# Performance work log

Measured on AMD Instinct MI355X. Metric: run time of the kernel, lower is better.

## Reference

```python
import jax, jax.numpy as jnp
import numpy as np

NEG = -1e9  # stand-in for -inf in masked_fill; avoids NaN rows for never-gathered states


def _residual(x, w1, b1, w2, b2):
    # ResidualLayerOld: two relu linears with a residual connection (eval mode, no dropout)
    h = jax.nn.relu(x @ w1.T + b1)
    return x + jax.nn.relu(h @ w2.T + b2)


def setup_inputs() -> dict:
    key = jax.random.key(0)
    B, T, V, C, H, SPW = 16, 256, 32000, 1024, 512, 8
    ks = jax.random.split(key, 32)
    s = 0.05  # keep logits in a sane range
    inp = {
        'start_emb': jax.random.normal(ks[0], (C, H), jnp.float32) * s,
        'start_l1w': jax.random.normal(ks[1], (H, H), jnp.float32) * s,
        'start_l1b': jnp.zeros((H,), jnp.float32),
        'start_l2w': jax.random.normal(ks[2], (H, H), jnp.float32) * s,
        'start_l2b': jnp.zeros((H,), jnp.float32),
        'start_ow': jax.random.normal(ks[3], (1, H), jnp.float32) * s,
        'start_ob': jnp.zeros((1,), jnp.float32),
        'state_emb': jax.random.normal(ks[4], (C, H), jnp.float32) * s,
        'trans_l1w': jax.random.normal(ks[5], (H, H), jnp.float32) * s,
        'trans_l1b': jnp.zeros((H,), jnp.float32),
        'trans_l2w': jax.random.normal(ks[6], (H, H), jnp.float32) * s,
        'trans_l2b': jnp.zeros((H,), jnp.float32),
        'proj_w': jax.random.normal(ks[7], (C, H), jnp.float32) * s,
        'pret_emb': jax.random.normal(ks[8], (C, H), jnp.float32) * s,
        'term_l1w': jax.random.normal(ks[9], (H, H), jnp.float32) * s,
        'term_l1b': jnp.zeros((H,), jnp.float32),
        'term_l2w': jax.random.normal(ks[10], (H, H), jnp.float32) * s,
        'term_l2b': jnp.zeros((H,), jnp.float32),
        'term_ow': jax.random.normal(ks[11], (V, H), jnp.float32) * s,
        'term_ob': jnp.zeros((V,), jnp.float32),
        'text': jax.random.randint(ks[12], (B, T), 0, V, jnp.int32),
        'word2state': jax.random.randint(ks[13], (V, SPW), 0, C, jnp.int32),
    }
    return inp


def reference(start_emb, start_l1w, start_l1b, start_l2w, start_l2b, start_ow, start_ob,
              state_emb, trans_l1w, trans_l1b, trans_l2w, trans_l2b, proj_w,
              pret_emb, term_l1w, term_l1b, term_l2w, term_l2b, term_ow, term_ob,
              text, word2state):
    C, H = start_emb.shape
    V, SPW = word2state.shape

    # start: MLP(C,H)->(C,1) -> log_softmax over C
    start = jax.nn.log_softmax(
        (_residual(start_emb, start_l1w, start_l1b, start_l2w, start_l2b) @ start_ow.T + start_ob).squeeze(-1))

    # transition: [C,C] log_softmax over next state
    trans = jax.nn.log_softmax(
        _residual(state_emb, trans_l1w, trans_l1b, trans_l2w, trans_l2b) @ proj_w.T, axis=-1)

    # emission: [C,V] logits, masked to the sparse word->state assignment, log_softmax over V
    term_logits = _residual(pret_emb, term_l1w, term_l1b, term_l2w, term_l2b) @ term_ow.T + term_ob
    mask = jnp.zeros((C, V), bool).at[word2state.reshape(-1), jnp.repeat(jnp.arange(V), SPW)].set(True)
    emission = jax.nn.log_softmax(jnp.where(mask, term_logits, NEG), axis=-1)

    # clamp: gather per-timestep [SPW,SPW] transition blocks + emissions
    cs = word2state[text]                               # [B,T,SPW]
    pot = trans[cs[:, :-1, :, None], cs[:, 1:, None, :]]  # [B,T-1,SPW,SPW] (prev i, next j)
    init = start[cs[:, 0]]                              # [B,SPW]
    obs = emission[cs, text[:, :, None]]                # [B,T,SPW]
    pot = pot.at[:, 0].add((init + obs[:, 0])[:, :, None])
    pot = pot + obs[:, 1:][:, :, None, :]               # add obs_{t+1} along next-state j
    pot = jnp.swapaxes(pot, -1, -2)                     # [B,T-1,next,prev], as in clamp()

    # forward algorithm (fb kernel's alpha pass): alpha_{t+1}[n] = LSE_p pot[t,n,p] + alpha_t[p]
    def step(alpha, p):
        a = jax.nn.logsumexp(p + alpha[:, None, :], axis=-1)
        return a, None

    B = text.shape[0]
    alpha0 = jnp.zeros((B, SPW), pot.dtype)
    alphaT, _ = jax.lax.scan(step, alpha0, jnp.swapaxes(pot, 0, 1))
    evidence = jax.nn.logsumexp(alphaT, axis=-1).sum()  # full-length sequences
    return evidence
```

## Files before the change

kernel.cpp:

```cpp
#include <hip/hip_runtime.h>
#include <hip/hip_bf16.h>

#define C_DIM 1024
#define H_DIM 512
#define V_DIM 32000
#define B_DIM 16
#define T_DIM 256
#define SPW   8
#define NSLOT 32

typedef unsigned short u16;
typedef unsigned int   u32;
typedef __attribute__((ext_vector_type(8))) short bf16x8;
typedef __attribute__((ext_vector_type(4))) float f32x4;

__device__ __forceinline__ u16 f2b(float f) {
    union { float f; u32 i; } x; x.f = f;
    u32 i = x.i;
    i += 0x7fffu + ((i >> 16) & 1u);
    return (u16)(i >> 16);
}
__device__ __forceinline__ float b2f(u16 u) {
    union { u32 i; float f; } x; x.i = ((u32)u) << 16; return x.f;
}
__device__ __forceinline__ float dot8_bf16(uint4 u, const float4 tw0, const float4 tw1) {
    return tw0.x * b2f((u16)(u.x & 0xffff)) + tw0.y * b2f((u16)(u.x >> 16))
         + tw0.z * b2f((u16)(u.y & 0xffff)) + tw0.w * b2f((u16)(u.y >> 16))
         + tw1.x * b2f((u16)(u.z & 0xffff)) + tw1.y * b2f((u16)(u.z >> 16))
         + tw1.z * b2f((u16)(u.w & 0xffff)) + tw1.w * b2f((u16)(u.w >> 16));
}

struct CvtArgs {
    const float* src[10];
    u16*         dst[10];
    int          n[10];
    float*       zero;
    int          zn;
};

__global__ __launch_bounds__(256) void cvt_kern(CvtArgs a)
{
    int seg = blockIdx.y;
    if (seg == 10) {
        for (int i = blockIdx.x * 256 + threadIdx.x; i < a.zn; i += gridDim.x * 256)
            a.zero[i] = 0.0f;
        return;
    }
    const float4* s = (const float4*)a.src[seg];
    ushort4* d = (ushort4*)a.dst[seg];
    int n4 = a.n[seg] >> 2;
    for (int i = blockIdx.x * 256 + threadIdx.x; i < n4; i += gridDim.x * 256) {
        float4 v = s[i];
        ushort4 o;
        o.x = f2b(v.x); o.y = f2b(v.y); o.z = f2b(v.z); o.w = f2b(v.w);
        d[i] = o;
    }
}

struct Mlp16Args {
    const u16*   A[3];
    const u16*   W[3];
    const float* bias[3];
    const u16*   resid[3];
    u16*         out[3];
};

__global__ __launch_bounds__(256) void mlp16_kern(Mlp16Args args)
{
    const int N = H_DIM, K = H_DIM;
    int z = blockIdx.z;
    const u16* A = args.A[z];
    const u16* B = args.W[z];
    const float* bias = args.bias[z];
    const u16* resid = args.resid[z];
    u16* out = args.out[z];

    __shared__ __align__(16) u16 As[64][40];
    __shared__ __align__(16) u16 Bs[64][40];
    int tid  = threadIdx.x;
    int m0 = blockIdx.x * 64, n0 = blockIdx.y * 64;
    int wave = tid >> 6, lane = tid & 63;
    int wr = wave >> 1, wc = wave & 1;
    int srow = tid >> 2, scol = (tid & 3) << 3;
    int quad = lane >> 4, l16 = lane & 15;
    f32x4 acc[2][2] = {};

    for (int k0 = 0; k0 < K; k0 += 32) {
        uint4 av = *(const uint4*)(A + (size_t)(m0 + srow) * K + k0 + scol);
        uint4 bv = *(const uint4*)(B + (size_t)(n0 + srow) * K + k0 + scol);
        __syncthreads();
        *(uint4*)&As[srow][scol] = av;
        *(uint4*)&Bs[srow][scol] = bv;
        __syncthreads();
        bf16x8 af0 = *(const bf16x8*)&As[wr * 32 + l16][quad * 8];
        bf16x8 af1 = *(const bf16x8*)&As[wr * 32 + 16 + l16][quad * 8];
        bf16x8 bf0 = *(const bf16x8*)&Bs[wc * 32 + l16][quad * 8];
        bf16x8 bf1 = *(const bf16x8*)&Bs[wc * 32 + 16 + l16][quad * 8];
        acc[0][0] = __builtin_amdgcn_mfma_f32_16x16x32_bf16(af0, bf0, acc[0][0], 0, 0, 0);
        acc[0][1] = __builtin_amdgcn_mfma_f32_16x16x32_bf16(af0, bf1, acc[0][1], 0, 0, 0);
        acc[1][0] = __builtin_amdgcn_mfma_f32_16x16x32_bf16(af1, bf0, acc[1][0], 0, 0, 0);
        acc[1][1] = __builtin_amdgcn_mfma_f32_16x16x32_bf16(af1, bf1, acc[1][1], 0, 0, 0);
    }
#pragma unroll
    for (int sm = 0; sm < 2; sm++)
#pragma unroll
        for (int sn = 0; sn < 2; sn++) {
            int n = n0 + wc * 32 + sn * 16 + l16;
            float bv = bias[n];
#pragma unroll
            for (int reg = 0; reg < 4; reg++) {
                int m = m0 + wr * 32 + sm * 16 + quad * 4 + reg;
                float v = fmaxf(acc[sm][sn][reg] + bv, 0.0f);
                if (resid) v += b2f(resid[(size_t)m * N + n]);
                out[(size_t)m * N + n] = f2b(v);
            }
        }
}

__global__ __launch_bounds__(256) void gemm16_kern(
    const u16* __restrict__ A, const u16* __restrict__ B,
    float* __restrict__ out, int M, int N, int K)
{
    __shared__ __align__(16) u16 As[64][40];
    __shared__ __align__(16) u16 Bs[64][40];
    int tid  = threadIdx.x;
    int m0 = blockIdx.x * 64, n0 = blockIdx.y * 64;
    int wave = tid >> 6, lane = tid & 63;
    int wr = wave >> 1, wc = wave & 1;
    int srow = tid >> 2, scol = (tid & 3) << 3;
    int quad = lane >> 4, l16 = lane & 15;
    f32x4 acc[2][2] = {};

    for (int k0 = 0; k0 < K; k0 += 32) {
        uint4 av = *(const uint4*)(A + (size_t)(m0 + srow) * K + k0 + scol);
        uint4 bv = *(const uint4*)(B + (size_t)(n0 + srow) * K + k0 + scol);
        __syncthreads();
        *(uint4*)&As[srow][scol] = av;
        *(uint4*)&Bs[srow][scol] = bv;
        __syncthreads();
        bf16x8 af0 = *(const bf16x8*)&As[wr * 32 + l16][quad * 8];
        bf16x8 af1 = *(const bf16x8*)&As[wr * 32 + 16 + l16][quad * 8];
        bf16x8 bf0 = *(const bf16x8*)&Bs[wc * 32 + l16][quad * 8];
        bf16x8 bf1 = *(const bf16x8*)&Bs[wc * 32 + 16 + l16][quad * 8];
        acc[0][0] = __builtin_amdgcn_mfma_f32_16x16x32_bf16(af0, bf0, acc[0][0], 0, 0, 0);
        acc[0][1] = __builtin_amdgcn_mfma_f32_16x16x32_bf16(af0, bf1, acc[0][1], 0, 0, 0);
        acc[1][0] = __builtin_amdgcn_mfma_f32_16x16x32_bf16(af1, bf0, acc[1][0], 0, 0, 0);
        acc[1][1] = __builtin_amdgcn_mfma_f32_16x16x32_bf16(af1, bf1, acc[1][1], 0, 0, 0);
    }
#pragma unroll
    for (int sm = 0; sm < 2; sm++)
#pragma unroll
        for (int sn = 0; sn < 2; sn++) {
            int n = n0 + wc * 32 + sn * 16 + l16;
#pragma unroll
            for (int reg = 0; reg < 4; reg++) {
                int m = m0 + wr * 32 + sm * 16 + quad * 4 + reg;
                out[(size_t)m * N + n] = acc[sm][sn][reg];
            }
        }
}

__global__ __launch_bounds__(256) void startlog_kern(
    const u16* __restrict__ Rstart16, const float* __restrict__ sow,
    const float* __restrict__ sob, float* __restrict__ startv,
    float* __restrict__ Ssum)
{
    int wid = threadIdx.x >> 6, lane = threadIdx.x & 63;
    int c = blockIdx.x * 4 + wid;
    uint4 rv = ((const uint4*)(Rstart16 + (size_t)c * H_DIM))[lane];
    const float4* wp = (const float4*)(sow);
    float4 w0 = wp[lane * 2], w1 = wp[lane * 2 + 1];
    float d = dot8_bf16(rv, w0, w1);
    for (int off = 1; off < 64; off <<= 1) d += __shfl_xor(d, off, 64);
    if (lane == 0) {
        d += sob[0];
        startv[c] = d;
        atomicAdd(Ssum + (blockIdx.x & (NSLOT - 1)), expf(d));
    }
}

__global__ __launch_bounds__(256) void rowlse_kern(const float* __restrict__ TL,
                                                   float* __restrict__ rowlse)
{
    int wid = threadIdx.x >> 6, lane = threadIdx.x & 63;
    int row = blockIdx.x * 4 + wid;
    const float4* p = (const float4*)(TL + (size_t)row * C_DIM);
    float s = 0.0f;
#pragma unroll
    for (int k = 0; k < 4; k++) {
        float4 v = p[lane + 64 * k];
        s += expf(v.x) + expf(v.y) + expf(v.z) + expf(v.w);
    }
    for (int off = 1; off < 64; off <<= 1) s += __shfl_xor(s, off, 64);
    if (lane == 0) rowlse[row] = logf(s);
}

__global__ __launch_bounds__(256) void zsum_kern(
    const u16* __restrict__ Rterm16, const float* __restrict__ tow,
    const float* __restrict__ tob, const int* __restrict__ w2s,
    float* __restrict__ Zpart)
{
    int wid = threadIdx.x >> 6, lane = threadIdx.x & 63;
    int v = blockIdx.x * 4 + wid;
    float* slot = Zpart + (blockIdx.x & (NSLOT - 1)) * C_DIM;
    const float4* twp = (const float4*)(tow + (size_t)v * H_DIM);
    float4 tw0 = twp[lane * 2], tw1 = twp[lane * 2 + 1];
    float ob = tob[v];
    int cs[SPW];
#pragma unroll
    for (int s = 0; s < SPW; s++) cs[s] = w2s[v * SPW + s];
    uint4 rv[SPW];
#pragma unroll
    for (int s = 0; s < SPW; s++)
        rv[s] = ((const uint4*)(Rterm16 + (size_t)cs[s] * H_DIM))[lane];
    float d[SPW];
#pragma unroll
    for (int s = 0; s < SPW; s++) {
        d[s] = dot8_bf16(rv[s], tw0, tw1);
        d[s] += __shfl_xor(d[s], 1, 64);
        d[s] += __shfl_xor(d[s], 2, 64);
        d[s] += __shfl_xor(d[s], 4, 64);
    }
    float x = d[0];
    int myc = cs[0];
#pragma unroll
    for (int s = 1; s < SPW; s++) {
        if ((lane & 7) == s) { x = d[s]; myc = cs[s]; }
    }
    x += __shfl_xor(x, 8, 64);
    x += __shfl_xor(x, 16, 64);
    x += __shfl_xor(x, 32, 64);
    u32 dupmask = 0;
#pragma unroll
    for (int s = 1; s < SPW; s++) {
        bool dp = false;
#pragma unroll
        for (int s2 = 0; s2 < s; s2++) dp = dp || (cs[s2] == cs[s]);
        if (dp) dupmask |= (1u << s);
    }
    if (lane < 8 && !((dupmask >> lane) & 1u))
        atomicAdd(slot + myc, expf(x + ob));
}

__global__ __launch_bounds__(256) void obs_kern(
    const u16* __restrict__ Rterm16, const float* __restrict__ tow,
    const float* __restrict__ tob, const int* __restrict__ w2s,
    const int* __restrict__ text, const float* __restrict__ Zpart,
    float* __restrict__ obs)
{
    int wid = threadIdx.x >> 6, lane = threadIdx.x & 63;
    int idx = blockIdx.x * 4 + wid;
    int v = text[idx];
    const float4* twp = (const float4*)(tow + (size_t)v * H_DIM);
    float4 tw0 = twp[lane * 2], tw1 = twp[lane * 2 + 1];
    float ob = tob[v];
    int cs[SPW];
#pragma unroll
    for (int s = 0; s < SPW; s++) cs[s] = w2s[v * SPW + s];
    uint4 rv[SPW];
#pragma unroll
    for (int s = 0; s < SPW; s++)
        rv[s] = ((const uint4*)(Rterm16 + (size_t)cs[s] * H_DIM))[lane];
    float d[SPW];
#pragma unroll
    for (int s = 0; s < SPW; s++) {
        d[s] = dot8_bf16(rv[s], tw0, tw1);
        d[s] += __shfl_xor(d[s], 1, 64);
        d[s] += __shfl_xor(d[s], 2, 64);
        d[s] += __shfl_xor(d[s], 4, 64);
    }
    float x = d[0];
    int myc = cs[0];
#pragma unroll
    for (int s = 1; s < SPW; s++) {
        if ((lane & 7) == s) { x = d[s]; myc = cs[s]; }
    }
    x += __shfl_xor(x, 8, 64);
    x += __shfl_xor(x, 16, 64);
    x += __shfl_xor(x, 32, 64);
    int g = lane >> 3;
    float zp = 0.0f;
#pragma unroll
    for (int k = 0; k < 4; k++)
        zp += Zpart[(size_t)(g * 4 + k) * C_DIM + myc];
    zp += __shfl_xor(zp, 8, 64);
    zp += __shfl_xor(zp, 16, 64);
    zp += __shfl_xor(zp, 32, 64);
    if (lane < 8)
        obs[idx * SPW + lane] = x + ob - logf(zp);
}

__device__ __forceinline__ float lsm_combine(float accv, float mv, int i, int j)
{
    float x[8];
#pragma unroll
    for (int k = 0; k < 8; k++) {
        float a = __shfl(accv, k * 8 + i, 64);
        float b = __shfl(mv,  j * 8 + k, 64);
        x[k] = a + b;
    }
    float mx = fmaxf(fmaxf(fmaxf(x[0], x[1]), fmaxf(x[2], x[3])),
                     fmaxf(fmaxf(x[4], x[5]), fmaxf(x[6], x[7])));
    float s = 0.0f;
#pragma unroll
    for (int k = 0; k < 8; k++) s += expf(x[k] - mx);
    return mx + logf(s);
}

__global__ __launch_bounds__(256) void scanA_kern(
    const float* __restrict__ TL, const float* __restrict__ rowlse,
    const float* __restrict__ obs, const float* __restrict__ startv,
    const float* __restrict__ Ssum, const int* __restrict__ text,
    const int* __restrict__ w2s, float* __restrict__ Mc)
{
    int wid = threadIdx.x >> 6, lane = threadIdx.x & 63;
    int g = blockIdx.x * 4 + wid;
    int b = g >> 4, c = g & 15;
    int t0 = c * 16;
    int cnt = min(16, (T_DIM - 1) - t0);
    int i = lane & 7, j = lane >> 3;

    const int* txt = text + b * T_DIM;
    const float* obsb = obs + (size_t)b * T_DIM * SPW;

    float logS = 0.0f;
    if (t0 == 0) {
        float ss = 0.0f;
#pragma unroll
        for (int k = 0; k < NSLOT; k++) ss += Ssum[k];
        logS = logf(ss);
    }

    auto potval = [&](int t) -> float {
        int vt  = txt[t];
        int vt1 = txt[t + 1];
        int ci = w2s[vt * SPW + i];
        int cj = w2s[vt1 * SPW + j];
        float p = TL[(size_t)ci * C_DIM + cj] - rowlse[ci] + obsb[(t + 1) * SPW + j];
        if (t == 0) p += startv[ci] - logS + obsb[i];
        return p;
    };

    float acc = potval(t0);
    if (cnt > 1) {
        float nv = potval(t0 + 1);
        for (int t = t0 + 1; t < t0 + cnt; t++) {
            float nv2 = (t + 1 < t0 + cnt) ? potval(t + 1) : 0.0f;
            acc = lsm_combine(acc, nv, i, j);
            nv = nv2;
        }
    }
    Mc[(size_t)g * 64 + lane] = acc;
}

__global__ __launch_bounds__(1024) void scanB_kern(const float* __restrict__ Mc,
                                                   float* __restrict__ out)
{
    int wave = threadIdx.x >> 6, lane = threadIdx.x & 63;
    int i = lane & 7, j = lane >> 3;
    const float* base = Mc + (size_t)wave * 16 * 64;
    float acc = base[lane];
    for (int c = 1; c < 16; c++)
        acc = lsm_combine(acc, base[(size_t)c * 64 + lane], i, j);
    float mx = acc;
    for (int o = 1; o < 64; o <<= 1) mx = fmaxf(mx, __shfl_xor(mx, o, 64));
    float e = expf(acc - mx);
    for (int o = 1; o < 64; o <<= 1) e += __shfl_xor(e, o, 64);
    __shared__ float part[16];
    if (lane == 0) part[wave] = mx + logf(e);
    __syncthreads();
    if (threadIdx.x == 0) {
        float s = 0.0f;
#pragma unroll
        for (int k = 0; k < 16; k++) s += part[k];
        out[0] = s;
    }
}

extern "C" void kernel_launch(void* const* d_in, const int* in_sizes, int n_in,
                              void* d_out, int out_size, void* d_ws, size_t ws_size,
                              hipStream_t stream)
{
    const float* start_emb = (const float*)d_in[0];
    const float* start_l1w = (const float*)d_in[1];
    const float* start_l1b = (const float*)d_in[2];
    const float* start_l2w = (const float*)d_in[3];
    const float* start_l2b = (const float*)d_in[4];
    const float* start_ow  = (const float*)d_in[5];
    const float* start_ob  = (const float*)d_in[6];
    const float* state_emb = (const float*)d_in[7];
    const float* trans_l1w = (const float*)d_in[8];
    const float* trans_l1b = (const float*)d_in[9];
    const float* trans_l2w = (const float*)d_in[10];
    const float* trans_l2b = (const float*)d_in[11];
    const float* proj_w    = (const float*)d_in[12];
    const float* pret_emb  = (const float*)d_in[13];
    const float* term_l1w  = (const float*)d_in[14];
    const float* term_l1b  = (const float*)d_in[15];
    const float* term_l2w  = (const float*)d_in[16];
    const float* term_l2b  = (const float*)d_in[17];
    const float* term_ow   = (const float*)d_in[18];
    const float* term_ob   = (const float*)d_in[19];
    const int*   text      = (const int*)d_in[20];
    const int*   w2s       = (const int*)d_in[21];

    char* w = (char*)d_ws;
    const u32 MB = 1u << 20;
    const size_t CH = (size_t)C_DIM * H_DIM;
    const size_t HH = (size_t)H_DIM * H_DIM;

    u16* emb16   = (u16*)(w);
    u16* w16     = (u16*)(w + 3u * MB);
    u16* proj16  = (u16*)(w + 6u * MB);
    u16* H16     = (u16*)(w + 7u * MB);
    u16* R16     = (u16*)(w + 10u * MB);
    float* TL    = (float*)(w + 13u * MB);
    float* startv  = (float*)(w + 17u * MB);
    float* rowlse  = (float*)(w + 17u * MB + 4096);
    float* obs     = (float*)(w + 17u * MB + 8192);
    float* Mc      = (float*)(w + 17u * MB + 8192 + 131072);
    float* Zpart   = (float*)(w + 18u * MB);
    float* Ssum    = Zpart + (size_t)NSLOT * C_DIM;

    u16* semb16 = emb16;
    u16* temb16 = emb16 + CH;
    u16* pemb16 = emb16 + 2 * CH;
    u16* sl1w16 = w16;
    u16* sl2w16 = w16 + HH;
    u16* tl1w16 = w16 + 2 * HH;
    u16* tl2w16 = w16 + 3 * HH;
    u16* ml1w16 = w16 + 4 * HH;
    u16* ml2w16 = w16 + 5 * HH;
    u16* Hs = H16, *Ht = H16 + CH, *Hp = H16 + 2 * CH;
    u16* Rstart16 = R16;
    u16* Rtrans16 = R16 + CH;
    u16* Rterm16  = R16 + 2 * CH;

    dim3 blk256(256);

    CvtArgs cv;
    cv.src[0] = start_emb; cv.dst[0] = semb16; cv.n[0] = (int)CH;
    cv.src[1] = state_emb; cv.dst[1] = temb16; cv.n[1] = (int)CH;
    cv.src[2] = pret_emb;  cv.dst[2] = pemb16; cv.n[2] = (int)CH;
    cv.src[3] = start_l1w; cv.dst[3] = sl1w16; cv.n[3] = (int)HH;
    cv.src[4] = start_l2w; cv.dst[4] = sl2w16; cv.n[4] = (int)HH;
    cv.src[5] = trans_l1w; cv.dst[5] = tl1w16; cv.n[5] = (int)HH;
    cv.src[6] = trans_l2w; cv.dst[6] = tl2w16; cv.n[6] = (int)HH;
    cv.src[7] = term_l1w;  cv.dst[7] = ml1w16; cv.n[7] = (int)HH;
    cv.src[8] = term_l2w;  cv.dst[8] = ml2w16; cv.n[8] = (int)HH;
    cv.src[9] = proj_w;    cv.dst[9] = proj16; cv.n[9] = (int)CH;
    cv.zero = Zpart; cv.zn = NSLOT * C_DIM + NSLOT;
    cvt_kern<<<dim3(128, 11), blk256, 0, stream>>>(cv);

    Mlp16Args l1 = {{semb16, temb16, pemb16},
                    {sl1w16, tl1w16, ml1w16},
                    {start_l1b, trans_l1b, term_l1b},
                    {nullptr, nullptr, nullptr},
                    {Hs, Ht, Hp}};
    Mlp16Args l2 = {{Hs, Ht, Hp},
                    {sl2w16, tl2w16, ml2w16},
                    {start_l2b, trans_l2b, term_l2b},
                    {semb16, temb16, pemb16},
                    {Rstart16, Rtrans16, Rterm16}};
    mlp16_kern<<<dim3(16, 8, 3), blk256, 0, stream>>>(l1);
    mlp16_kern<<<dim3(16, 8, 3), blk256, 0, stream>>>(l2);

    gemm16_kern<<<dim3(16, 16), blk256, 0, stream>>>(Rtrans16, proj16, TL,
                                                     C_DIM, C_DIM, H_DIM);

    startlog_kern<<<C_DIM / 4, blk256, 0, stream>>>(Rstart16, start_ow, start_ob,
                                                    startv, Ssum);
    zsum_kern<<<V_DIM / 4, blk256, 0, stream>>>(Rterm16, term_ow, term_ob, w2s, Zpart);
    rowlse_kern<<<C_DIM / 4, blk256, 0, stream>>>(TL, rowlse);
    obs_kern<<<B_DIM * T_DIM / 4, blk256, 0, stream>>>(Rterm16, term_ow, term_ob, w2s,
                                                       text, Zpart, obs);
    scanA_kern<<<B_DIM * 16 / 4, blk256, 0, stream>>>(TL, rowlse, obs, startv, Ssum,
                                                      text, w2s, Mc);
    scanB_kern<<<1, 1024, 0, stream>>>(Mc, (float*)d_out);
}
```

Before: 240.6 us.

## Fuse whole pipeline into one cooperative persistent kernel with grid syncs

Replaces the chain of about ten kernel launches with a single cooperative persistent kernel that runs conversion, both MLP layers, the projection GEMM, normalizers and the chunked scan as phases separated by grid.sync. The row-logsumexp is folded into the projection GEMM epilogue through atomic partial sums. The start/transition-projection work runs on half the blocks while the other half computes the emission partition, so the stages overlap. This removes launch gaps and a separate pass over TL, at the cost of grid-wide barriers, lower per-phase parallelism, and a fallback path if the cooperative launch fails.

```diff
diff --git a/kernel.cpp b/kernel.cpp
--- a/kernel.cpp
+++ b/kernel.cpp
@@ -1,5 +1,8 @@
 #include <hip/hip_runtime.h>
+#include <hip/hip_cooperative_groups.h>
 #include <hip/hip_bf16.h>
+
+namespace cg = cooperative_groups;
 
 #define C_DIM 1024
 #define H_DIM 512
@@ -30,64 +33,50 @@
          + tw1.z * b2f((u16)(u.w & 0xffff)) + tw1.w * b2f((u16)(u.w >> 16));
 }
 
-struct CvtArgs {
-    const float* src[10];
-    u16*         dst[10];
-    int          n[10];
-    float*       zero;
-    int          zn;
-};
-
-__global__ __launch_bounds__(256) void cvt_kern(CvtArgs a)
-{
-    int seg = blockIdx.y;
-    if (seg == 10) {
-        for (int i = blockIdx.x * 256 + threadIdx.x; i < a.zn; i += gridDim.x * 256)
-            a.zero[i] = 0.0f;
-        return;
-    }
-    const float4* s = (const float4*)a.src[seg];
-    ushort4* d = (ushort4*)a.dst[seg];
-    int n4 = a.n[seg] >> 2;
-    for (int i = blockIdx.x * 256 + threadIdx.x; i < n4; i += gridDim.x * 256) {
-        float4 v = s[i];
-        ushort4 o;
-        o.x = f2b(v.x); o.y = f2b(v.y); o.z = f2b(v.z); o.w = f2b(v.w);
-        d[i] = o;
-    }
-}
-
-struct Mlp16Args {
-    const u16*   A[3];
-    const u16*   W[3];
-    const float* bias[3];
-    const u16*   resid[3];
-    u16*         out[3];
-};
-
-__global__ __launch_bounds__(256) void mlp16_kern(Mlp16Args args)
-{
-    const int N = H_DIM, K = H_DIM;
-    int z = blockIdx.z;
-    const u16* A = args.A[z];
-    const u16* B = args.W[z];
-    const float* bias = args.bias[z];
-    const u16* resid = args.resid[z];
-    u16* out = args.out[z];
-
-    __shared__ __align__(16) u16 As[64][40];
-    __shared__ __align__(16) u16 Bs[64][40];
-    int tid  = threadIdx.x;
-    int m0 = blockIdx.x * 64, n0 = blockIdx.y * 64;
+__device__ __forceinline__ float sparse8_dot(
+    const u16* __restrict__ Rterm16, const float* __restrict__ tow,
+    const int* __restrict__ w2s, int v, int lane, int* csOut, int* mycOut)
+{
+    const float4* twp = (const float4*)(tow + (size_t)v * H_DIM);
+    float4 tw0 = twp[lane * 2], tw1 = twp[lane * 2 + 1];
+#pragma unroll
+    for (int s = 0; s < SPW; s++) csOut[s] = w2s[v * SPW + s];
+    uint4 rv[SPW];
+#pragma unroll
+    for (int s = 0; s < SPW; s++)
+        rv[s] = ((const uint4*)(Rterm16 + (size_t)csOut[s] * H_DIM))[lane];
+    float d[SPW];
+#pragma unroll
+    for (int s = 0; s < SPW; s++) {
+        d[s] = dot8_bf16(rv[s], tw0, tw1);
+        d[s] += __shfl_xor(d[s], 1, 64);
+        d[s] += __shfl_xor(d[s], 2, 64);
+        d[s] += __shfl_xor(d[s], 4, 64);
+    }
+    float x = d[0];
+    int myc = csOut[0];
+#pragma unroll
+    for (int s = 1; s < SPW; s++)
+        if ((lane & 7) == s) { x = d[s]; myc = csOut[s]; }
+    x += __shfl_xor(x, 8, 64);
+    x += __shfl_xor(x, 16, 64);
+    x += __shfl_xor(x, 32, 64);
+    *mycOut = myc;
+    return x;
+}
+
+__device__ __forceinline__ void gemm_tile_acc(
+    const u16* __restrict__ A, const u16* __restrict__ Bw,
+    int m0, int n0, int tid, u16 As[64][40], u16 Bs[64][40], f32x4 acc[2][2])
+{
+    const int K = H_DIM;
+    int srow = tid >> 2, scol = (tid & 3) << 3;
     int wave = tid >> 6, lane = tid & 63;
     int wr = wave >> 1, wc = wave & 1;
-    int srow = tid >> 2, scol = (tid & 3) << 3;
     int quad = lane >> 4, l16 = lane & 15;
-    f32x4 acc[2][2] = {};
-
     for (int k0 = 0; k0 < K; k0 += 32) {
         uint4 av = *(const uint4*)(A + (size_t)(m0 + srow) * K + k0 + scol);
-        uint4 bv = *(const uint4*)(B + (size_t)(n0 + srow) * K + k0 + scol);
+        uint4 bv = *(const uint4*)(Bw + (size_t)(n0 + srow) * K + k0 + scol);
         __syncthreads();
         *(uint4*)&As[srow][scol] = av;
         *(uint4*)&Bs[srow][scol] = bv;
@@ -101,6 +90,342 @@
         acc[1][0] = __builtin_amdgcn_mfma_f32_16x16x32_bf16(af1, bf0, acc[1][0], 0, 0, 0);
         acc[1][1] = __builtin_amdgcn_mfma_f32_16x16x32_bf16(af1, bf1, acc[1][1], 0, 0, 0);
     }
+}
+
+__device__ __forceinline__ float lsm_combine(float accv, float mv, int i, int j)
+{
+    float x[8];
+#pragma unroll
+    for (int k = 0; k < 8; k++) {
+        float a = __shfl(accv, k * 8 + i, 64);
+        float b = __shfl(mv,  j * 8 + k, 64);
+        x[k] = a + b;
+    }
+    float mx = fmaxf(fmaxf(fmaxf(x[0], x[1]), fmaxf(x[2], x[3])),
+                     fmaxf(fmaxf(x[4], x[5]), fmaxf(x[6], x[7])));
+    float s = 0.0f;
+#pragma unroll
+    for (int k = 0; k < 8; k++) s += expf(x[k] - mx);
+    return mx + logf(s);
+}
+
+struct MegaArgs {
+    const float *start_emb, *start_l1b, *start_l2b, *start_ow, *start_ob;
+    const float *state_emb, *trans_l1b, *trans_l2b;
+    const float *pret_emb, *term_l1b, *term_l2b, *term_ow, *term_ob;
+    const float *srcw[10];
+    const int *text, *w2s;
+    u16 *emb16, *w16, *proj16, *H16, *R16;
+    float *TL, *startv, *rowlse, *logZ, *logS, *Mc, *Zpart, *rowZ, *Ssum;
+    float *zeroBase;
+    int zeroCount;
+    float *out;
+};
+
+__global__ __launch_bounds__(256, 2) void mega_kern(MegaArgs a)
+{
+    cg::grid_group grid = cg::this_grid();
+    __shared__ __align__(16) u16 As[64][40];
+    __shared__ __align__(16) u16 Bs[64][40];
+    __shared__ float part[16];
+
+    const size_t CH = (size_t)C_DIM * H_DIM;
+    const size_t HH = (size_t)H_DIM * H_DIM;
+    int tid = threadIdx.x;
+    int bid = blockIdx.x;
+    int nb = gridDim.x;
+    int gtid = bid * 256 + tid;
+    int gsz = nb * 256;
+    int wid = tid >> 6, lane = tid & 63;
+    int wr = wid >> 1, wc = wid & 1;
+    int quad = lane >> 4, l16 = lane & 15;
+
+    {
+        u16* dst[10] = {a.emb16, a.emb16 + CH, a.emb16 + 2 * CH,
+                        a.w16, a.w16 + HH, a.w16 + 2 * HH,
+                        a.w16 + 3 * HH, a.w16 + 4 * HH, a.w16 + 5 * HH, a.proj16};
+        int n4[10] = {(int)(CH / 4), (int)(CH / 4), (int)(CH / 4),
+                      (int)(HH / 4), (int)(HH / 4), (int)(HH / 4),
+                      (int)(HH / 4), (int)(HH / 4), (int)(HH / 4), (int)(CH / 4)};
+        for (int seg = 0; seg < 10; seg++) {
+            const float4* s = (const float4*)a.srcw[seg];
+            ushort4* dd = (ushort4*)dst[seg];
+            int n = n4[seg];
+            for (int idx = gtid; idx < n; idx += gsz) {
+                float4 v = s[idx];
+                ushort4 o;
+                o.x = f2b(v.x); o.y = f2b(v.y); o.z = f2b(v.z); o.w = f2b(v.w);
+                dd[idx] = o;
+            }
+        }
+        for (int idx = gtid; idx < a.zeroCount; idx += gsz)
+            a.zeroBase[idx] = 0.0f;
+    }
+    __threadfence();
+    grid.sync();
+
+    for (int tile = bid; tile < 384; tile += nb) {
+        int z = tile >> 7, r = tile & 127;
+        int m0 = (r & 15) * 64, n0 = (r >> 4) * 64;
+        const u16* A = a.emb16 + (size_t)z * CH;
+        const u16* W = a.w16 + (size_t)(2 * z) * HH;
+        const float* bias = (z == 0) ? a.start_l1b : (z == 1) ? a.trans_l1b : a.term_l1b;
+        u16* out = a.H16 + (size_t)z * CH;
+        f32x4 acc[2][2] = {};
+        gemm_tile_acc(A, W, m0, n0, tid, As, Bs, acc);
+#pragma unroll
+        for (int sm = 0; sm < 2; sm++)
+#pragma unroll
+            for (int sn = 0; sn < 2; sn++) {
+                int n = n0 + wc * 32 + sn * 16 + l16;
+                float bv = bias[n];
+#pragma unroll
+                for (int reg = 0; reg < 4; reg++) {
+                    int m = m0 + wr * 32 + sm * 16 + quad * 4 + reg;
+                    out[(size_t)m * H_DIM + n] = f2b(fmaxf(acc[sm][sn][reg] + bv, 0.0f));
+                }
+            }
+    }
+    __threadfence();
+    grid.sync();
+
+    for (int tile = bid; tile < 384; tile += nb) {
+        int z = tile >> 7, r = tile & 127;
+        int m0 = (r & 15) * 64, n0 = (r >> 4) * 64;
+        const u16* A = a.H16 + (size_t)z * CH;
+        const u16* W = a.w16 + (size_t)(2 * z + 1) * HH;
+        const float* bias = (z == 0) ? a.start_l2b : (z == 1) ? a.trans_l2b : a.term_l2b;
+        const u16* resid = a.emb16 + (size_t)z * CH;
+        u16* out = a.R16 + (size_t)z * CH;
+        f32x4 acc[2][2] = {};
+        gemm_tile_acc(A, W, m0, n0, tid, As, Bs, acc);
+#pragma unroll
+        for (int sm = 0; sm < 2; sm++)
+#pragma unroll
+            for (int sn = 0; sn < 2; sn++) {
+                int n = n0 + wc * 32 + sn * 16 + l16;
+                float bv = bias[n];
+#pragma unroll
+                for (int reg = 0; reg < 4; reg++) {
+                    int m = m0 + wr * 32 + sm * 16 + quad * 4 + reg;
+                    float v = fmaxf(acc[sm][sn][reg] + bv, 0.0f)
+                            + b2f(resid[(size_t)m * H_DIM + n]);
+                    out[(size_t)m * H_DIM + n] = f2b(v);
+                }
+            }
+    }
+    __threadfence();
+    grid.sync();
+
+    {
+        int half = nb >> 1;
+        if (bid < half) {
+            for (int tile = bid; tile < 256; tile += half) {
+                int m0 = (tile & 15) * 64, n0 = (tile >> 4) * 64;
+                int slot = tile >> 4;
+                f32x4 acc[2][2] = {};
+                gemm_tile_acc(a.R16 + CH, a.proj16, m0, n0, tid, As, Bs, acc);
+#pragma unroll
+                for (int sm = 0; sm < 2; sm++)
+#pragma unroll
+                    for (int reg = 0; reg < 4; reg++) {
+                        int m = m0 + wr * 32 + sm * 16 + quad * 4 + reg;
+                        float e2 = 0.0f;
+#pragma unroll
+                        for (int sn = 0; sn < 2; sn++) {
+                            int n = n0 + wc * 32 + sn * 16 + l16;
+                            float v = acc[sm][sn][reg];
+                            a.TL[(size_t)m * C_DIM + n] = v;
+                            e2 += expf(v);
+                        }
+                        e2 += __shfl_xor(e2, 1, 64);
+                        e2 += __shfl_xor(e2, 2, 64);
+                        e2 += __shfl_xor(e2, 4, 64);
+                        e2 += __shfl_xor(e2, 8, 64);
+                        if (l16 == 0)
+                            atomicAdd(&a.rowZ[(size_t)slot * C_DIM + m], e2);
+                    }
+            }
+            for (int c = bid * 4 + wid; c < C_DIM; c += half * 4) {
+                uint4 rv = ((const uint4*)(a.R16 + (size_t)c * H_DIM))[lane];
+                const float4* wp = (const float4*)(a.start_ow);
+                float4 w0 = wp[lane * 2], w1 = wp[lane * 2 + 1];
+                float d = dot8_bf16(rv, w0, w1);
+                for (int off = 1; off < 64; off <<= 1) d += __shfl_xor(d, off, 64);
+                if (lane == 0) {
+                    d += a.start_ob[0];
+                    a.startv[c] = d;
+                    atomicAdd(&a.Ssum[c & (NSLOT - 1)], expf(d));
+                }
+            }
+        } else {
+            const u16* Rterm16 = a.R16 + 2 * CH;
+            int nw = (nb - half) * 4;
+            float* slot = a.Zpart + (size_t)(bid & (NSLOT - 1)) * C_DIM;
+#pragma unroll 1
+            for (int v = (bid - half) * 4 + wid; v < V_DIM; v += nw) {
+                int cs[SPW], myc;
+                float x = sparse8_dot(Rterm16, a.term_ow, a.w2s, v, lane, cs, &myc);
+                float ob = a.term_ob[v];
+                u32 dupmask = 0;
+#pragma unroll
+                for (int s = 1; s < SPW; s++) {
+                    bool dp = false;
+#pragma unroll
+                    for (int s2 = 0; s2 < s; s2++) dp = dp || (cs[s2] == cs[s]);
+                    if (dp) dupmask |= (1u << s);
+                }
+                if (lane < 8 && !((dupmask >> lane) & 1u))
+                    atomicAdd(slot + myc, expf(x + ob));
+            }
+        }
+    }
+    __threadfence();
+    grid.sync();
+
+    for (int idx = gtid; idx < 2 * C_DIM + 1; idx += gsz) {
+        if (idx < C_DIM) {
+            float s = 0.0f;
+#pragma unroll
+            for (int k = 0; k < NSLOT; k++) s += a.Zpart[(size_t)k * C_DIM + idx];
+            a.logZ[idx] = logf(s);
+        } else if (idx < 2 * C_DIM) {
+            int r = idx - C_DIM;
+            float s = 0.0f;
+#pragma unroll
+            for (int k = 0; k < 16; k++) s += a.rowZ[(size_t)k * C_DIM + r];
+            a.rowlse[r] = logf(s);
+        } else {
+            float s = 0.0f;
+#pragma unroll
+            for (int k = 0; k < NSLOT; k++) s += a.Ssum[k];
+            a.logS[0] = logf(s);
+        }
+    }
+    __threadfence();
+    grid.sync();
+
+    for (int g = bid * 4 + wid; g < 256; g += nb * 4) {
+        const u16* Rterm16 = a.R16 + 2 * CH;
+        int b = g >> 4, c = g & 15;
+        int t0 = c * 16;
+        int cnt = min(16, (T_DIM - 1) - t0);
+        int i = lane & 7, j = lane >> 3;
+        const int* txt = a.text + b * T_DIM;
+
+        float ov[17];
+#pragma unroll
+        for (int k = 0; k < 17; k++) {
+            if (k <= cnt) {
+                int v = txt[t0 + k];
+                int cs[SPW], myc;
+                float x = sparse8_dot(Rterm16, a.term_ow, a.w2s, v, lane, cs, &myc);
+                ov[k] = x + a.term_ob[v] - a.logZ[myc];
+            } else ov[k] = 0.0f;
+        }
+        float acc;
+        {
+            int vt = txt[t0], vt1 = txt[t0 + 1];
+            int ci = a.w2s[vt * SPW + i];
+            int cj = a.w2s[vt1 * SPW + j];
+            float p = a.TL[(size_t)ci * C_DIM + cj] - a.rowlse[ci]
+                    + __shfl(ov[1], j, 64);
+            if (t0 == 0) p += a.startv[ci] - a.logS[0] + __shfl(ov[0], i, 64);
+            acc = p;
+        }
+#pragma unroll
+        for (int k = 1; k < 16; k++) {
+            if (k < cnt) {
+                int t = t0 + k;
+                int vt = txt[t], vt1 = txt[t + 1];
+                int ci = a.w2s[vt * SPW + i];
+                int cj = a.w2s[vt1 * SPW + j];
+                float p = a.TL[(size_t)ci * C_DIM + cj] - a.rowlse[ci]
+                        + __shfl(ov[k + 1], j, 64);
+                acc = lsm_combine(acc, p, i, j);
+            }
+        }
+        a.Mc[(size_t)g * 64 + lane] = acc;
+    }
+    __threadfence();
+    grid.sync();
+
+    if (bid == 0) {
+        int i = lane & 7, j = lane >> 3;
+        for (int b = wid; b < B_DIM; b += 4) {
+            const float* base = a.Mc + (size_t)b * 16 * 64;
+            float acc = base[lane];
+            for (int c = 1; c < 16; c++)
+                acc = lsm_combine(acc, base[(size_t)c * 64 + lane], i, j);
+            float mx = acc;
+            for (int o = 1; o < 64; o <<= 1) mx = fmaxf(mx, __shfl_xor(mx, o, 64));
+            float e = expf(acc - mx);
+            for (int o = 1; o < 64; o <<= 1) e += __shfl_xor(e, o, 64);
+            if (lane == 0) part[b] = mx + logf(e);
+        }
+        __syncthreads();
+        if (tid == 0) {
+            float s = 0.0f;
+#pragma unroll
+            for (int k = 0; k < B_DIM; k++) s += part[k];
+            a.out[0] = s;
+        }
+    }
+}
+
+struct CvtArgs {
+    const float* src[10];
+    u16*         dst[10];
+    int          n[10];
+    float*       zero;
+    int          zn;
+};
+
+__global__ __launch_bounds__(256) void fb_cvt(CvtArgs a)
+{
+    int seg = blockIdx.y;
+    if (seg == 10) {
+        for (int i = blockIdx.x * 256 + threadIdx.x; i < a.zn; i += gridDim.x * 256)
+            a.zero[i] = 0.0f;
+        return;
+    }
+    const float4* s = (const float4*)a.src[seg];
+    ushort4* d = (ushort4*)a.dst[seg];
+    int n4 = a.n[seg] >> 2;
+    for (int i = blockIdx.x * 256 + threadIdx.x; i < n4; i += gridDim.x * 256) {
+        float4 v = s[i];
+        ushort4 o;
+        o.x = f2b(v.x); o.y = f2b(v.y); o.z = f2b(v.z); o.w = f2b(v.w);
+        d[i] = o;
+    }
+}
+
+struct Mlp16Args {
+    const u16*   A[3];
+    const u16*   W[3];
+    const float* bias[3];
+    const u16*   resid[3];
+    u16*         out[3];
+};
+
+__global__ __launch_bounds__(256) void fb_mlp(Mlp16Args args)
+{
+    const int N = H_DIM;
+    int z = blockIdx.z;
+    const u16* A = args.A[z];
+    const u16* W = args.W[z];
+    const float* bias = args.bias[z];
+    const u16* resid = args.resid[z];
+    u16* out = args.out[z];
+    __shared__ __align__(16) u16 As[64][40];
+    __shared__ __align__(16) u16 Bs[64][40];
+    int tid = threadIdx.x;
+    int m0 = blockIdx.x * 64, n0 = blockIdx.y * 64;
+    int wave = tid >> 6, lane = tid & 63;
+    int wr = wave >> 1, wc = wave & 1;
+    int quad = lane >> 4, l16 = lane & 15;
+    f32x4 acc[2][2] = {};
+    gemm_tile_acc(A, W, m0, n0, tid, As, Bs, acc);
 #pragma unroll
     for (int sm = 0; sm < 2; sm++)
 #pragma unroll
@@ -117,36 +442,18 @@
         }
 }
 
-__global__ __launch_bounds__(256) void gemm16_kern(
-    const u16* __restrict__ A, const u16* __restrict__ B,
-    float* __restrict__ out, int M, int N, int K)
+__global__ __launch_bounds__(256) void fb_gemm(
+    const u16* __restrict__ A, const u16* __restrict__ B, float* __restrict__ out)
 {
     __shared__ __align__(16) u16 As[64][40];
     __shared__ __align__(16) u16 Bs[64][40];
-    int tid  = threadIdx.x;
+    int tid = threadIdx.x;
     int m0 = blockIdx.x * 64, n0 = blockIdx.y * 64;
     int wave = tid >> 6, lane = tid & 63;
     int wr = wave >> 1, wc = wave & 1;
-    int srow = tid >> 2, scol = (tid & 3) << 3;
     int quad = lane >> 4, l16 = lane & 15;
     f32x4 acc[2][2] = {};
-
-    for (int k0 = 0; k0 < K; k0 += 32) {
-        uint4 av = *(const uint4*)(A + (size_t)(m0 + srow) * K + k0 + scol);
-        uint4 bv = *(const uint4*)(B + (size_t)(n0 + srow) * K + k0 + scol);
-        __syncthreads();
-        *(uint4*)&As[srow][scol] = av;
-        *(uint4*)&Bs[srow][scol] = bv;
-        __syncthreads();
-        bf16x8 af0 = *(const bf16x8*)&As[wr * 32 + l16][quad * 8];
-        bf16x8 af1 = *(const bf16x8*)&As[wr * 32 + 16 + l16][quad * 8];
-        bf16x8 bf0 = *(const bf16x8*)&Bs[wc * 32 + l16][quad * 8];
-        bf16x8 bf1 = *(const bf16x8*)&Bs[wc * 32 + 16 + l16][quad * 8];
-        acc[0][0] = __builtin_amdgcn_mfma_f32_16x16x32_bf16(af0, bf0, acc[0][0], 0, 0, 0);
-        acc[0][1] = __builtin_amdgcn_mfma_f32_16x16x32_bf16(af0, bf1, acc[0][1], 0, 0, 0);
-        acc[1][0] = __builtin_amdgcn_mfma_f32_16x16x32_bf16(af1, bf0, acc[1][0], 0, 0, 0);
-        acc[1][1] = __builtin_amdgcn_mfma_f32_16x16x32_bf16(af1, bf1, acc[1][1], 0, 0, 0);
-    }
+    gemm_tile_acc(A, B, m0, n0, tid, As, Bs, acc);
 #pragma unroll
     for (int sm = 0; sm < 2; sm++)
 #pragma unroll
@@ -155,12 +462,12 @@
 #pragma unroll
             for (int reg = 0; reg < 4; reg++) {
                 int m = m0 + wr * 32 + sm * 16 + quad * 4 + reg;
-                out[(size_t)m * N + n] = acc[sm][sn][reg];
-            }
-        }
-}
-
-__global__ __launch_bounds__(256) void startlog_kern(
+                out[(size_t)m * C_DIM + n] = acc[sm][sn][reg];
+            }
+        }
+}
+
+__global__ __launch_bounds__(256) void fb_startlog(
     const u16* __restrict__ Rstart16, const float* __restrict__ sow,
     const float* __restrict__ sob, float* __restrict__ startv,
     float* __restrict__ Ssum)
@@ -179,8 +486,8 @@
     }
 }
 
-__global__ __launch_bounds__(256) void rowlse_kern(const float* __restrict__ TL,
-                                                   float* __restrict__ rowlse)
+__global__ __launch_bounds__(256) void fb_rowlse(const float* __restrict__ TL,
+                                                 float* __restrict__ rowlse)
 {
     int wid = threadIdx.x >> 6, lane = threadIdx.x & 63;
     int row = blockIdx.x * 4 + wid;
@@ -195,41 +502,17 @@
     if (lane == 0) rowlse[row] = logf(s);
 }
 
-__global__ __launch_bounds__(256) void zsum_kern(
+__global__ __launch_bounds__(256) void fb_zsum(
     const u16* __restrict__ Rterm16, const float* __restrict__ tow,
     const float* __restrict__ tob, const int* __restrict__ w2s,
     float* __restrict__ Zpart)
 {
     int wid = threadIdx.x >> 6, lane = threadIdx.x & 63;
     int v = blockIdx.x * 4 + wid;
-    float* slot = Zpart + (blockIdx.x & (NSLOT - 1)) * C_DIM;
-    const float4* twp = (const float4*)(tow + (size_t)v * H_DIM);
-    float4 tw0 = twp[lane * 2], tw1 = twp[lane * 2 + 1];
+    float* slot = Zpart + (size_t)(blockIdx.x & (NSLOT - 1)) * C_DIM;
+    int cs[SPW], myc;
+    float x = sparse8_dot(Rterm16, tow, w2s, v, lane, cs, &myc);
     float ob = tob[v];
-    int cs[SPW];
-#pragma unroll
-    for (int s = 0; s < SPW; s++) cs[s] = w2s[v * SPW + s];
-    uint4 rv[SPW];
-#pragma unroll
-    for (int s = 0; s < SPW; s++)
-        rv[s] = ((const uint4*)(Rterm16 + (size_t)cs[s] * H_DIM))[lane];
-    float d[SPW];
-#pragma unroll
-    for (int s = 0; s < SPW; s++) {
-        d[s] = dot8_bf16(rv[s], tw0, tw1);
-        d[s] += __shfl_xor(d[s], 1, 64);
-        d[s] += __shfl_xor(d[s], 2, 64);
-        d[s] += __shfl_xor(d[s], 4, 64);
-    }
-    float x = d[0];
-    int myc = cs[0];
-#pragma unroll
-    for (int s = 1; s < SPW; s++) {
-        if ((lane & 7) == s) { x = d[s]; myc = cs[s]; }
-    }
-    x += __shfl_xor(x, 8, 64);
-    x += __shfl_xor(x, 16, 64);
-    x += __shfl_xor(x, 32, 64);
     u32 dupmask = 0;
 #pragma unroll
     for (int s = 1; s < SPW; s++) {
@@ -242,7 +525,7 @@
         atomicAdd(slot + myc, expf(x + ob));
 }
 
-__global__ __launch_bounds__(256) void obs_kern(
+__global__ __launch_bounds__(256) void fb_obs(
     const u16* __restrict__ Rterm16, const float* __restrict__ tow,
     const float* __restrict__ tob, const int* __restrict__ w2s,
     const int* __restrict__ text, const float* __restrict__ Zpart,
@@ -251,33 +534,9 @@
     int wid = threadIdx.x >> 6, lane = threadIdx.x & 63;
     int idx = blockIdx.x * 4 + wid;
     int v = text[idx];
-    const float4* twp = (const float4*)(tow + (size_t)v * H_DIM);
-    float4 tw0 = twp[lane * 2], tw1 = twp[lane * 2 + 1];
+    int cs[SPW], myc;
+    float x = sparse8_dot(Rterm16, tow, w2s, v, lane, cs, &myc);
     float ob = tob[v];
-    int cs[SPW];
-#pragma unroll
-    for (int s = 0; s < SPW; s++) cs[s] = w2s[v * SPW + s];
-    uint4 rv[SPW];
-#pragma unroll
-    for (int s = 0; s < SPW; s++)
-        rv[s] = ((const uint4*)(Rterm16 + (size_t)cs[s] * H_DIM))[lane];
-    float d[SPW];
-#pragma unroll
-    for (int s = 0; s < SPW; s++) {
-        d[s] = dot8_bf16(rv[s], tw0, tw1);
-        d[s] += __shfl_xor(d[s], 1, 64);
-        d[s] += __shfl_xor(d[s], 2, 64);
-        d[s] += __shfl_xor(d[s], 4, 64);
-    }
-    float x = d[0];
-    int myc = cs[0];
-#pragma unroll
-    for (int s = 1; s < SPW; s++) {
-        if ((lane & 7) == s) { x = d[s]; myc = cs[s]; }
-    }
-    x += __shfl_xor(x, 8, 64);
-    x += __shfl_xor(x, 16, 64);
-    x += __shfl_xor(x, 32, 64);
     int g = lane >> 3;
     float zp = 0.0f;
 #pragma unroll
@@ -290,24 +549,7 @@
         obs[idx * SPW + lane] = x + ob - logf(zp);
 }
 
-__device__ __forceinline__ float lsm_combine(float accv, float mv, int i, int j)
-{
-    float x[8];
-#pragma unroll
-    for (int k = 0; k < 8; k++) {
-        float a = __shfl(accv, k * 8 + i, 64);
-        float b = __shfl(mv,  j * 8 + k, 64);
-        x[k] = a + b;
-    }
-    float mx = fmaxf(fmaxf(fmaxf(x[0], x[1]), fmaxf(x[2], x[3])),
-                     fmaxf(fmaxf(x[4], x[5]), fmaxf(x[6], x[7])));
-    float s = 0.0f;
-#pragma unroll
-    for (int k = 0; k < 8; k++) s += expf(x[k] - mx);
-    return mx + logf(s);
-}
-
-__global__ __launch_bounds__(256) void scanA_kern(
+__global__ __launch_bounds__(256) void fb_scanA(
     const float* __restrict__ TL, const float* __restrict__ rowlse,
     const float* __restrict__ obs, const float* __restrict__ startv,
     const float* __restrict__ Ssum, const int* __restrict__ text,
@@ -319,10 +561,8 @@
     int t0 = c * 16;
     int cnt = min(16, (T_DIM - 1) - t0);
     int i = lane & 7, j = lane >> 3;
-
     const int* txt = text + b * T_DIM;
     const float* obsb = obs + (size_t)b * T_DIM * SPW;
-
     float logS = 0.0f;
     if (t0 == 0) {
         float ss = 0.0f;
@@ -330,34 +570,26 @@
         for (int k = 0; k < NSLOT; k++) ss += Ssum[k];
         logS = logf(ss);
     }
-
     auto potval = [&](int t) -> float {
-        int vt  = txt[t];
-        int vt1 = txt[t + 1];
+        int vt = txt[t], vt1 = txt[t + 1];
         int ci = w2s[vt * SPW + i];
         int cj = w2s[vt1 * SPW + j];
         float p = TL[(size_t)ci * C_DIM + cj] - rowlse[ci] + obsb[(t + 1) * SPW + j];
         if (t == 0) p += startv[ci] - logS + obsb[i];
         return p;
     };
-
     float acc = potval(t0);
-    if (cnt > 1) {
-        float nv = potval(t0 + 1);
-        for (int t = t0 + 1; t < t0 + cnt; t++) {
-            float nv2 = (t + 1 < t0 + cnt) ? potval(t + 1) : 0.0f;
-            acc = lsm_combine(acc, nv, i, j);
-            nv = nv2;
-        }
-    }
+    for (int t = t0 + 1; t < t0 + cnt; t++)
+        acc = lsm_combine(acc, potval(t), i, j);
     Mc[(size_t)g * 64 + lane] = acc;
 }
 
-__global__ __launch_bounds__(1024) void scanB_kern(const float* __restrict__ Mc,
-                                                   float* __restrict__ out)
+__global__ __launch_bounds__(1024) void fb_scanB(const float* __restrict__ Mc,
+                                                 float* __restrict__ out)
 {
     int wave = threadIdx.x >> 6, lane = threadIdx.x & 63;
     int i = lane & 7, j = lane >> 3;
+    __shared__ float part[16];
     const float* base = Mc + (size_t)wave * 16 * 64;
     float acc = base[lane];
     for (int c = 1; c < 16; c++)
@@ -366,13 +598,12 @@
     for (int o = 1; o < 64; o <<= 1) mx = fmaxf(mx, __shfl_xor(mx, o, 64));
     float e = expf(acc - mx);
     for (int o = 1; o < 64; o <<= 1) e += __shfl_xor(e, o, 64);
-    __shared__ float part[16];
     if (lane == 0) part[wave] = mx + logf(e);
     __syncthreads();
     if (threadIdx.x == 0) {
         float s = 0.0f;
 #pragma unroll
-        for (int k = 0; k < 16; k++) s += part[k];
+        for (int k = 0; k < B_DIM; k++) s += part[k];
         out[0] = s;
     }
 }
@@ -381,100 +612,117 @@
                               void* d_out, int out_size, void* d_ws, size_t ws_size,
                               hipStream_t stream)
 {
-    const float* start_emb = (const float*)d_in[0];
-    const float* start_l1w = (const float*)d_in[1];
-    const float* start_l1b = (const float*)d_in[2];
-    const float* start_l2w = (const float*)d_in[3];
-    const float* start_l2b = (const float*)d_in[4];
-    const float* start_ow  = (const float*)d_in[5];
-    const float* start_ob  = (const float*)d_in[6];
-    const float* state_emb = (const float*)d_in[7];
-    const float* trans_l1w = (const float*)d_in[8];
-    const float* trans_l1b = (const float*)d_in[9];
-    const float* trans_l2w = (const float*)d_in[10];
-    const float* trans_l2b = (const float*)d_in[11];
-    const float* proj_w    = (const float*)d_in[12];
-    const float* pret_emb  = (const float*)d_in[13];
-    const float* term_l1w  = (const float*)d_in[14];
-    const float* term_l1b  = (const float*)d_in[15];
-    const float* term_l2w  = (const float*)d_in[16];
-    const float* term_l2b  = (const float*)d_in[17];
-    const float* term_ow   = (const float*)d_in[18];
-    const float* term_ob   = (const float*)d_in[19];
-    const int*   text      = (const int*)d_in[20];
-    const int*   w2s       = (const int*)d_in[21];
-
     char* w = (char*)d_ws;
     const u32 MB = 1u << 20;
     const size_t CH = (size_t)C_DIM * H_DIM;
     const size_t HH = (size_t)H_DIM * H_DIM;
 
-    u16* emb16   = (u16*)(w);
-    u16* w16     = (u16*)(w + 3u * MB);
-    u16* proj16  = (u16*)(w + 6u * MB);
-    u16* H16     = (u16*)(w + 7u * MB);
-    u16* R16     = (u16*)(w + 10u * MB);
-    float* TL    = (float*)(w + 13u * MB);
-    float* startv  = (float*)(w + 17u * MB);
-    float* rowlse  = (float*)(w + 17u * MB + 4096);
-    float* obs     = (float*)(w + 17u * MB + 8192);
-    float* Mc      = (float*)(w + 17u * MB + 8192 + 131072);
-    float* Zpart   = (float*)(w + 18u * MB);
-    float* Ssum    = Zpart + (size_t)NSLOT * C_DIM;
-
-    u16* semb16 = emb16;
-    u16* temb16 = emb16 + CH;
-    u16* pemb16 = emb16 + 2 * CH;
-    u16* sl1w16 = w16;
-    u16* sl2w16 = w16 + HH;
-    u16* tl1w16 = w16 + 2 * HH;
-    u16* tl2w16 = w16 + 3 * HH;
-    u16* ml1w16 = w16 + 4 * HH;
-    u16* ml2w16 = w16 + 5 * HH;
-    u16* Hs = H16, *Ht = H16 + CH, *Hp = H16 + 2 * CH;
-    u16* Rstart16 = R16;
-    u16* Rtrans16 = R16 + CH;
-    u16* Rterm16  = R16 + 2 * CH;
-
+    MegaArgs a;
+    a.start_emb = (const float*)d_in[0];
+    a.start_l1b = (const float*)d_in[2];
+    a.start_l2b = (const float*)d_in[4];
+    a.start_ow  = (const float*)d_in[5];
+    a.start_ob  = (const float*)d_in[6];
+    a.state_emb = (const float*)d_in[7];
+    a.trans_l1b = (const float*)d_in[9];
+    a.trans_l2b = (const float*)d_in[11];
+    a.pret_emb  = (const float*)d_in[13];
+    a.term_l1b  = (const float*)d_in[15];
+    a.term_l2b  = (const float*)d_in[17];
+    a.term_ow   = (const float*)d_in[18];
+    a.term_ob   = (const float*)d_in[19];
+    a.text      = (const int*)d_in[20];
+    a.w2s       = (const int*)d_in[21];
+    a.srcw[0] = (const float*)d_in[0];
+    a.srcw[1] = (const float*)d_in[7];
+    a.srcw[2] = (const float*)d_in[13];
+    a.srcw[3] = (const float*)d_in[1];
+    a.srcw[4] = (const float*)d_in[3];
+    a.srcw[5] = (const float*)d_in[8];
+    a.srcw[6] = (const float*)d_in[10];
+    a.srcw[7] = (const float*)d_in[14];
+    a.srcw[8] = (const float*)d_in[16];
+    a.srcw[9] = (const float*)d_in[12];
+
+    a.emb16  = (u16*)(w);
+    a.w16    = (u16*)(w + 3u * MB);
+    a.proj16 = (u16*)(w + 6u * MB);
+    a.H16    = (u16*)(w + 7u * MB);
+    a.R16    = (u16*)(w + 10u * MB);
+    a.TL     = (float*)(w + 13u * MB);
+    a.startv = (float*)(w + 17u * MB);
+    a.rowlse = (float*)(w + 17u * MB + 4096);
+    a.logZ   = (float*)(w + 17u * MB + 8192);
+    a.logS   = (float*)(w + 17u * MB + 12288);
+    a.Mc     = (float*)(w + 17u * MB + 16384);
+    float* obs = (float*)(w + 17u * MB + 16384 + 65536);
+    a.Zpart  = (float*)(w + 18u * MB);
+    a.rowZ   = (float*)(w + 18u * MB + 131072);
+    a.Ssum   = (float*)(w + 18u * MB + 131072 + 65536);
+    a.zeroBase  = a.Zpart;
+    a.zeroCount = NSLOT * C_DIM + 16 * C_DIM + NSLOT;
+    a.out    = (float*)d_out;
+
+    int maxPerCU = 0;
+    hipError_t qe = hipOccupancyMaxActiveBlocksPerMultiprocessor(&maxPerCU,
+                                                                 mega_kern, 256, 0);
+    bool done = false;
+    if (qe == hipSuccess && maxPerCU >= 1) {
+        int nblk = maxPerCU * 256;
+        if (nblk > 512) nblk = 512;
+        if (nblk >= 16) {
+            void* kp[] = { &a };
+            if (hipLaunchCooperativeKernel(mega_kern, dim3(nblk), dim3(256),
+                                           kp, 0, stream) == hipSuccess)
+                done = true;
+        }
+    }
+    if (done) return;
+
+    u16* Hs = a.H16;
+    u16* Ht = a.H16 + CH;
+    u16* Hp = a.H16 + 2 * CH;
+    u16* Rstart16 = a.R16;
+    u16* Rtrans16 = a.R16 + CH;
+    u16* Rterm16  = a.R16 + 2 * CH;
     dim3 blk256(256);
 
     CvtArgs cv;
-    cv.src[0] = start_emb; cv.dst[0] = semb16; cv.n[0] = (int)CH;
-    cv.src[1] = state_emb; cv.dst[1] = temb16; cv.n[1] = (int)CH;
-    cv.src[2] = pret_emb;  cv.dst[2] = pemb16; cv.n[2] = (int)CH;
-    cv.src[3] = start_l1w; cv.dst[3] = sl1w16; cv.n[3] = (int)HH;
-    cv.src[4] = start_l2w; cv.dst[4] = sl2w16; cv.n[4] = (int)HH;
-    cv.src[5] = trans_l1w; cv.dst[5] = tl1w16; cv.n[5] = (int)HH;
-    cv.src[6] = trans_l2w; cv.dst[6] = tl2w16; cv.n[6] = (int)HH;
-    cv.src[7] = term_l1w;  cv.dst[7] = ml1w16; cv.n[7] = (int)HH;
-    cv.src[8] = term_l2w;  cv.dst[8] = ml2w16; cv.n[8] = (int)HH;
-    cv.src[9] = proj_w;    cv.dst[9] = proj16; cv.n[9] = (int)CH;
-    cv.zero = Zpart; cv.zn = NSLOT * C_DIM + NSLOT;
-    cvt_kern<<<dim3(128, 11), blk256, 0, stream>>>(cv);
-
-    Mlp16Args l1 = {{semb16, temb16, pemb16},
-                    {sl1w16, tl1w16, ml1w16},
-                    {start_l1b, trans_l1b, term_l1b},
+    for (int k = 0; k < 10; k++) cv.src[k] = a.srcw[k];
+    cv.dst[0] = a.emb16;          cv.n[0] = (int)CH;
+    cv.dst[1] = a.emb16 + CH;     cv.n[1] = (int)CH;
+    cv.dst[2] = a.emb16 + 2 * CH; cv.n[2] = (int)CH;
+    cv.dst[3] = a.w16;            cv.n[3] = (int)HH;
+    cv.dst[4] = a.w16 + HH;       cv.n[4] = (int)HH;
+    cv.dst[5] = a.w16 + 2 * HH;   cv.n[5] = (int)HH;
+    cv.dst[6] = a.w16 + 3 * HH;   cv.n[6] = (int)HH;
+    cv.dst[7] = a.w16 + 4 * HH;   cv.n[7] = (int)HH;
+    cv.dst[8] = a.w16 + 5 * HH;   cv.n[8] = (int)HH;
+    cv.dst[9] = a.proj16;         cv.n[9] = (int)CH;
+    cv.zero = a.zeroBase; cv.zn = a.zeroCount;
+    fb_cvt<<<dim3(128, 11), blk256, 0, stream>>>(cv);
+
+    Mlp16Args l1 = {{a.emb16, a.emb16 + CH, a.emb16 + 2 * CH},
+                    {a.w16, a.w16 + 2 * HH, a.w16 + 4 * HH},
+                    {a.start_l1b, a.trans_l1b, a.term_l1b},
                     {nullptr, nullptr, nullptr},
                     {Hs, Ht, Hp}};
     Mlp16Args l2 = {{Hs, Ht, Hp},
-                    {sl2w16, tl2w16, ml2w16},
-                    {start_l2b, trans_l2b, term_l2b},
-                    {semb16, temb16, pemb16},
+                    {a.w16 + HH, a.w16 + 3 * HH, a.w16 + 5 * HH},
+                    {a.start_l2b, a.trans_l2b, a.term_l2b},
+                    {a.emb16, a.emb16 + CH, a.emb16 + 2 * CH},
                     {Rstart16, Rtrans16, Rterm16}};
-    mlp16_kern<<<dim3(16, 8, 3), blk256, 0, stream>>>(l1);
-    mlp16_kern<<<dim3(16, 8, 3), blk256, 0, stream>>>(l2);
-
-    gemm16_kern<<<dim3(16, 16), blk256, 0, stream>>>(Rtrans16, proj16, TL,
-                                                     C_DIM, C_DIM, H_DIM);
-
-    startlog_kern<<<C_DIM / 4, blk256, 0, stream>>>(Rstart16, start_ow, start_ob,
-                                                    startv, Ssum);
-    zsum_kern<<<V_DIM / 4, blk256, 0, stream>>>(Rterm16, term_ow, term_ob, w2s, Zpart);
-    rowlse_kern<<<C_DIM / 4, blk256, 0, stream>>>(TL, rowlse);
-    obs_kern<<<B_DIM * T_DIM / 4, blk256, 0, stream>>>(Rterm16, term_ow, term_ob, w2s,
-                                                       text, Zpart, obs);
-    scanA_kern<<<B_DIM * 16 / 4, blk256, 0, stream>>>(TL, rowlse, obs, startv, Ssum,
-                                                      text, w2s, Mc);
-    scanB_kern<<<1, 1024, 0, stream>>>(Mc, (float*)d_out);
-}
+    fb_mlp<<<dim3(16, 8, 3), blk256, 0, stream>>>(l1);
+    fb_mlp<<<dim3(16, 8, 3), blk256, 0, stream>>>(l2);
+    fb_gemm<<<dim3(16, 16), blk256, 0, stream>>>(Rtrans16, a.proj16, a.TL);
+    fb_startlog<<<C_DIM / 4, blk256, 0, stream>>>(Rstart16, a.start_ow, a.start_ob,
+                                                  a.startv, a.Ssum);
+    fb_zsum<<<V_DIM / 4, blk256, 0, stream>>>(Rterm16, a.term_ow, a.term_ob,
+                                              a.w2s, a.Zpart);
+    fb_rowlse<<<C_DIM / 4, blk256, 0, stream>>>(a.TL, a.rowlse);
+    fb_obs<<<B_DIM * T_DIM / 4, blk256, 0, stream>>>(Rterm16, a.term_ow, a.term_ob,
+                                                     a.w2s, a.text, a.Zpart, obs);
+    fb_scanA<<<B_DIM * 16 / 4, blk256, 0, stream>>>(a.TL, a.rowlse, obs, a.startv,
+                                                    a.Ssum, a.text, a.w2s, a.Mc);
+    fb_scanB<<<1, 1024, 0, stream>>>(a.Mc, (float*)d_out);
+}
```

Result: slower. 696.6 us (+189.6%).
